# Kernel tuning notes

Hardware: AMD Instinct MI355X
Metric: run time of the kernel (lower is better)

## Reference

```python
import jax, jax.numpy as jnp
import numpy as np

N = 50000
IN_CH = 256
HID = 256
E = 800000


def setup_inputs() -> dict:
    key = jax.random.key(0)
    ks = jax.random.split(key, 12)
    s = 1.0 / np.sqrt(HID)
    return {
        "x": jax.random.normal(ks[0], (N, IN_CH), jnp.float32),
        "edge_index": jax.random.randint(ks[1], (2, E), 0, N, dtype=jnp.int64),
        "prev_embedding": jax.random.normal(ks[2], (N, HID), jnp.float32),
        "W1": jax.random.normal(ks[3], (IN_CH, HID), jnp.float32) / np.sqrt(IN_CH),
        "b1": jnp.zeros((HID,), jnp.float32),
        "W2": jax.random.normal(ks[4], (HID, HID), jnp.float32) * s,
        "b2": jnp.zeros((HID,), jnp.float32),
        "gWw": jax.random.normal(ks[5], (HID, HID), jnp.float32) * s,
        "gWb": jnp.zeros((HID,), jnp.float32),
        "gUw": jax.random.normal(ks[6], (HID, HID), jnp.float32) * s,
        "gUb": jnp.zeros((HID,), jnp.float32),
    }


def _gcn_conv(x, W, b, src, dst, norm):
    # PyG GCNConv: h = x @ W; out[i] = sum_j norm_ij * h[j]; + bias
    h = x @ W
    msg = h[src] * norm[:, None]  # [E+N, H]
    out = jax.ops.segment_sum(msg, dst, num_segments=N)
    return out + b


def _norm_and_loops(edge_index):
    loop = jnp.arange(N, dtype=edge_index.dtype)
    src = jnp.concatenate([edge_index[0], loop])
    dst = jnp.concatenate([edge_index[1], loop])
    deg = jax.ops.segment_sum(jnp.ones_like(dst, dtype=jnp.float32), dst, num_segments=N)
    dinv = jnp.where(deg > 0, jax.lax.rsqrt(deg), 0.0)
    norm = dinv[src] * dinv[dst]
    return src, dst, norm


def reference(x, edge_index, prev_embedding, W1, b1, W2, b2, gWw, gWb, gUw, gUb):
    src, dst, norm = _norm_and_loops(edge_index)
    h = jax.nn.relu(_gcn_conv(x, W1, b1, src, dst, norm))
    h_t = _gcn_conv(h, W2, b2, src, dst, norm)
    alpha = jax.nn.sigmoid(h_t @ gWw + gWb + prev_embedding @ gUw + gUb)
    h_tilde = alpha * h_t + (1.0 - alpha) * prev_embedding
    return (h_tilde, h_t)
```

## Files before the change

kernel.cpp:

```cpp
#include <hip/hip_runtime.h>
#include <hip/hip_bf16.h>
#include <math.h>

#define HIDC 256

typedef short short8 __attribute__((ext_vector_type(8)));
typedef float f32x4 __attribute__((ext_vector_type(4)));

__device__ __forceinline__ ushort f2bf_rne(float f) {
    uint u = __float_as_uint(f);
    u += 0x7FFF + ((u >> 16) & 1);
    return (ushort)(u >> 16);
}
__device__ __forceinline__ float bf2f(ushort h) {
    return __uint_as_float(((uint)h) << 16);
}

__device__ __forceinline__ short8 pack8_rne(float4 a, float4 b) {
    ushort h[8];
    h[0] = f2bf_rne(a.x); h[1] = f2bf_rne(a.y); h[2] = f2bf_rne(a.z); h[3] = f2bf_rne(a.w);
    h[4] = f2bf_rne(b.x); h[5] = f2bf_rne(b.y); h[6] = f2bf_rne(b.z); h[7] = f2bf_rne(b.w);
    return *(short8*)h;
}
__device__ __forceinline__ void split8(float4 a, float4 b, short8& hi, short8& lo) {
    float v[8] = {a.x, a.y, a.z, a.w, b.x, b.y, b.z, b.w};
    ushort hh[8], ll[8];
#pragma unroll
    for (int q = 0; q < 8; q++) {
        uint u = __float_as_uint(v[q]);
        hh[q] = (ushort)(u >> 16);
        ll[q] = f2bf_rne(v[q] - __uint_as_float(u & 0xFFFF0000u));
    }
    hi = *(short8*)hh; lo = *(short8*)ll;
}


__global__ void fill_i_kernel(int* __restrict__ p, int v, int n) {
    int i = blockIdx.x * 256 + threadIdx.x;
    if (i < n) p[i] = v;
}

__global__ void deg_kernel(const int* __restrict__ dst, int* __restrict__ deg, int E) {
    int e = blockIdx.x * 256 + threadIdx.x;
    if (e < E) atomicAdd(&deg[dst[e]], 1);
}

__global__ void rsqrt_kernel(const int* __restrict__ deg, float* __restrict__ dinv, int n) {
    int i = blockIdx.x * 256 + threadIdx.x;
    if (i < n) dinv[i] = rsqrtf((float)(deg[i] + 1));
}


__device__ __forceinline__ int block_incl_scan(int v, int tid) {
#pragma unroll
    for (int off = 1; off < 64; off <<= 1) {
        int t = __shfl_up(v, off);
        if ((tid & 63) >= off) v += t;
    }
    __shared__ int wt[4];
    if ((tid & 63) == 63) wt[tid >> 6] = v;
    __syncthreads();
    int wid = tid >> 6;
    for (int w = 0; w < wid; w++) v += wt[w];
    __syncthreads();
    return v;
}

__global__ void scan_a_kernel(const int* __restrict__ deg, int* __restrict__ row_start,
                              int* __restrict__ blocksum, int N) {
    int tid = threadIdx.x;
    int i = blockIdx.x * 256 + tid;
    int v = (i < N) ? deg[i] : 0;
    int incl = block_incl_scan(v, tid);
    if (i < N) row_start[i + 1] = incl;
    if (tid == 255) blocksum[blockIdx.x] = incl;
}

__global__ void scan_b_kernel(int* __restrict__ blocksum, int nb) {
    int tid = threadIdx.x;
    int v = (tid < nb) ? blocksum[tid] : 0;
    int incl = block_incl_scan(v, tid);
    if (tid < nb) blocksum[tid] = incl;
}

__global__ void scan_c_kernel(int* __restrict__ row_start, int* __restrict__ cursor,
                              const int* __restrict__ blocksum, int N) {
    int b = blockIdx.x;
    int i = b * 256 + threadIdx.x;
    int add = (b > 0) ? blocksum[b - 1] : 0;
    if (i < N) {
        int v = row_start[i + 1] + add;
        row_start[i + 1] = v;
        cursor[i + 1] = v;
    }
    if (b == 0 && threadIdx.x == 0) { row_start[0] = 0; cursor[0] = 0; }
}

__global__ void scatter_kernel(const int* __restrict__ src, const int* __restrict__ dst,
                               const float* __restrict__ dinv, int* __restrict__ cursor,
                               int* __restrict__ csr_src, float* __restrict__ csr_w, int E) {
    int e = blockIdx.x * 256 + threadIdx.x;
    if (e < E) {
        int s = src[e], d = dst[e];
        int pos = atomicAdd(&cursor[d], 1);
        csr_src[pos] = s;
        csr_w[pos] = dinv[s] * dinv[d];
    }
}


__global__ void prep_bt_kernel(const float* __restrict__ B, ushort* __restrict__ BF) {
    int n = blockIdx.x, k = threadIdx.x;
    ushort v = f2bf_rne(B[k * 256 + n]);
    int lane = ((k >> 3) & 3) * 16 + (n & 15);
    int idx = ((n >> 4) * 4096) + ((k >> 5) * 512) + lane * 8 + (k & 7);
    BF[idx] = v;
}

__global__ void prep_gate_bt_kernel(const float* __restrict__ gWw, const float* __restrict__ gUw,
                                    ushort* __restrict__ BhF, ushort* __restrict__ BlF) {
    int n = blockIdx.x, t = threadIdx.x;
#pragma unroll
    for (int p = 0; p < 2; p++) {
        int k = p * 256 + t;
        float v = (p ? gUw : gWw)[t * 256 + n];
        uint u = __float_as_uint(v);
        ushort hi = (ushort)(u >> 16);
        ushort lo = f2bf_rne(v - __uint_as_float(u & 0xFFFF0000u));
        int lane = ((k >> 3) & 3) * 16 + (n & 15);
        int idx = ((n >> 4) * 8192) + ((k >> 5) * 512) + lane * 8 + (k & 7);
        BhF[idx] = hi; BlF[idx] = lo;
    }
}


__global__ __launch_bounds__(256, 4) void gemm_bf16_kernel(
    const float* __restrict__ A, const ushort* __restrict__ BF,
    ushort* __restrict__ C, int M)
{
    const int tl = threadIdx.x;
    const int lane = tl & 63, wave = tl >> 6;
    const int wm = (wave & 1) * 32, wn = (wave >> 1) * 64;
    const int bm = blockIdx.x * 64, bn = blockIdx.y * 128;
    const int fr = lane & 15, kg = (lane >> 4) * 8;

    const int r0 = bm + wm + fr, r1 = r0 + 16;
    const bool ok0 = r0 < M, ok1 = r1 < M;
    const float* a0 = A + (size_t)r0 * HIDC + kg;
    const float* a1 = A + (size_t)r1 * HIDC + kg;
    const ushort* bp = BF + (size_t)((bn + wn) >> 4) * 4096 + lane * 8;

    f32x4 acc[2][4] = {};

    for (int kq = 0; kq < 8; kq++) {
        float4 z = make_float4(0.f, 0.f, 0.f, 0.f);
        float4 u0 = z, u1 = z, v0 = z, v1 = z;
        if (ok0) { u0 = *(const float4*)(a0 + kq * 32); u1 = *(const float4*)(a0 + kq * 32 + 4); }
        if (ok1) { v0 = *(const float4*)(a1 + kq * 32); v1 = *(const float4*)(a1 + kq * 32 + 4); }
        short8 af0 = pack8_rne(u0, u1);
        short8 af1 = pack8_rne(v0, v1);
        short8 bfv[4];
#pragma unroll
        for (int nt = 0; nt < 4; nt++)
            bfv[nt] = *(const short8*)(bp + ((size_t)nt * 8 + kq) * 512);
#pragma unroll
        for (int nt = 0; nt < 4; nt++) {
            acc[0][nt] = __builtin_amdgcn_mfma_f32_16x16x32_bf16(af0, bfv[nt], acc[0][nt], 0, 0, 0);
            acc[1][nt] = __builtin_amdgcn_mfma_f32_16x16x32_bf16(af1, bfv[nt], acc[1][nt], 0, 0, 0);
        }
    }

    const int row4 = (lane >> 4) * 4, coln = lane & 15;
#pragma unroll
    for (int mt = 0; mt < 2; mt++)
#pragma unroll
        for (int r = 0; r < 4; r++) {
            int m = bm + wm + mt * 16 + row4 + r;
            if (m < M) {
#pragma unroll
                for (int nt = 0; nt < 4; nt++) {
                    int n = bn + wn + nt * 16 + coln;
                    C[(size_t)m * HIDC + n] = f2bf_rne(acc[mt][nt][r]);
                }
            }
        }
}


__global__ __launch_bounds__(256, 4) void gemm_bf16A_kernel(
    const ushort* __restrict__ A, const ushort* __restrict__ BF,
    ushort* __restrict__ C, int M)
{
    const int tl = threadIdx.x;
    const int lane = tl & 63, wave = tl >> 6;
    const int wm = (wave & 1) * 32, wn = (wave >> 1) * 64;
    const int bm = blockIdx.x * 64, bn = blockIdx.y * 128;
    const int fr = lane & 15, kg = (lane >> 4) * 8;

    const int r0 = bm + wm + fr, r1 = r0 + 16;
    const bool ok0 = r0 < M, ok1 = r1 < M;
    const ushort* a0 = A + (size_t)r0 * HIDC + kg;
    const ushort* a1 = A + (size_t)r1 * HIDC + kg;
    const ushort* bp = BF + (size_t)((bn + wn) >> 4) * 4096 + lane * 8;

    f32x4 acc[2][4] = {};

    for (int kq = 0; kq < 8; kq++) {
        short8 af0 = {}, af1 = {};
        if (ok0) af0 = *(const short8*)(a0 + kq * 32);
        if (ok1) af1 = *(const short8*)(a1 + kq * 32);
        short8 bfv[4];
#pragma unroll
        for (int nt = 0; nt < 4; nt++)
            bfv[nt] = *(const short8*)(bp + ((size_t)nt * 8 + kq) * 512);
#pragma unroll
        for (int nt = 0; nt < 4; nt++) {
            acc[0][nt] = __builtin_amdgcn_mfma_f32_16x16x32_bf16(af0, bfv[nt], acc[0][nt], 0, 0, 0);
            acc[1][nt] = __builtin_amdgcn_mfma_f32_16x16x32_bf16(af1, bfv[nt], acc[1][nt], 0, 0, 0);
        }
    }

    const int row4 = (lane >> 4) * 4, coln = lane & 15;
#pragma unroll
    for (int mt = 0; mt < 2; mt++)
#pragma unroll
        for (int r = 0; r < 4; r++) {
            int m = bm + wm + mt * 16 + row4 + r;
            if (m < M) {
#pragma unroll
                for (int nt = 0; nt < 4; nt++) {
                    int n = bn + wn + nt * 16 + coln;
                    C[(size_t)m * HIDC + n] = f2bf_rne(acc[mt][nt][r]);
                }
            }
        }
}


__global__ __launch_bounds__(256, 4) void gate_kernel(
    const float* __restrict__ ht, const float* __restrict__ prev,
    const ushort* __restrict__ BhF, const ushort* __restrict__ BlF,
    const float* __restrict__ gWb, const float* __restrict__ gUb,
    float* __restrict__ out, int M)
{
    const int tl = threadIdx.x;
    const int lane = tl & 63, wave = tl >> 6;
    const int wm = (wave & 1) * 32, wn = (wave >> 1) * 64;
    const int bm = blockIdx.x * 64, bn = blockIdx.y * 128;
    const int fr = lane & 15, kg = (lane >> 4) * 8;

    const int r0 = bm + wm + fr, r1 = r0 + 16;
    const bool ok0 = r0 < M, ok1 = r1 < M;
    const size_t ro0 = (size_t)r0 * HIDC + kg;
    const size_t ro1 = (size_t)r1 * HIDC + kg;
    const ushort* bph = BhF + (size_t)((bn + wn) >> 4) * 8192 + lane * 8;
    const ushort* bpl = BlF + (size_t)((bn + wn) >> 4) * 8192 + lane * 8;

    f32x4 acc[2][4] = {};

    for (int kq = 0; kq < 16; kq++) {
        const float* S = (kq < 8) ? ht : prev;
        const int cb = (kq & 7) * 32;
        float4 z = make_float4(0.f, 0.f, 0.f, 0.f);
        float4 u0 = z, u1 = z, v0 = z, v1 = z;
        if (ok0) { u0 = *(const float4*)(S + ro0 + cb); u1 = *(const float4*)(S + ro0 + cb + 4); }
        if (ok1) { v0 = *(const float4*)(S + ro1 + cb); v1 = *(const float4*)(S + ro1 + cb + 4); }
        short8 ah0, al0, ah1, al1;
        split8(u0, u1, ah0, al0);
        split8(v0, v1, ah1, al1);
        short8 bfh[4], bfl[4];
#pragma unroll
        for (int nt = 0; nt < 4; nt++) {
            size_t off = ((size_t)nt * 16 + kq) * 512;
            bfh[nt] = *(const short8*)(bph + off);
            bfl[nt] = *(const short8*)(bpl + off);
        }
#pragma unroll
        for (int nt = 0; nt < 4; nt++) {
            acc[0][nt] = __builtin_amdgcn_mfma_f32_16x16x32_bf16(ah0, bfh[nt], acc[0][nt], 0, 0, 0);
            acc[0][nt] = __builtin_amdgcn_mfma_f32_16x16x32_bf16(ah0, bfl[nt], acc[0][nt], 0, 0, 0);
            acc[0][nt] = __builtin_amdgcn_mfma_f32_16x16x32_bf16(al0, bfh[nt], acc[0][nt], 0, 0, 0);
            acc[1][nt] = __builtin_amdgcn_mfma_f32_16x16x32_bf16(ah1, bfh[nt], acc[1][nt], 0, 0, 0);
            acc[1][nt] = __builtin_amdgcn_mfma_f32_16x16x32_bf16(ah1, bfl[nt], acc[1][nt], 0, 0, 0);
            acc[1][nt] = __builtin_amdgcn_mfma_f32_16x16x32_bf16(al1, bfh[nt], acc[1][nt], 0, 0, 0);
        }
    }

    const int row4 = (lane >> 4) * 4, coln = lane & 15;
#pragma unroll
    for (int mt = 0; mt < 2; mt++)
#pragma unroll
        for (int r = 0; r < 4; r++) {
            int m = bm + wm + mt * 16 + row4 + r;
            if (m < M) {
#pragma unroll
                for (int nt = 0; nt < 4; nt++) {
                    int n = bn + wn + nt * 16 + coln;
                    size_t idx = (size_t)m * HIDC + n;
                    float g = acc[mt][nt][r] + gWb[n] + gUb[n];
                    float alpha = 1.f / (1.f + expf(-g));
                    out[idx] = alpha * ht[idx] + (1.f - alpha) * prev[idx];
                }
            }
        }
}


__global__ __launch_bounds__(256) void csr_agg_kernel(
    const ushort* __restrict__ hm, const int* __restrict__ row_start,
    const int* __restrict__ csr_src, const float* __restrict__ csr_w,
    const float* __restrict__ dinv, const float* __restrict__ bias,
    float* __restrict__ outf, ushort* __restrict__ outb, int do_relu, int N)
{
    const int wave = threadIdx.x >> 6, lane = threadIdx.x & 63;
    const int i = blockIdx.x * 4 + wave;
    if (i >= N) return;
    const int c = lane * 4;

    const float di = dinv[i];
    const float s2 = di * di;
    ushort4 sv = *(const ushort4*)(hm + (size_t)i * HIDC + c);
    float a0 = s2 * bf2f(sv.x), a1 = s2 * bf2f(sv.y);
    float a2 = s2 * bf2f(sv.z), a3 = s2 * bf2f(sv.w);

    const int b0 = row_start[i], b1 = row_start[i + 1];
    int t = b0;
    for (; t + 4 <= b1; t += 4) {
        int   i0 = csr_src[t],     i1 = csr_src[t + 1];
        int   i2 = csr_src[t + 2], i3 = csr_src[t + 3];
        float w0 = csr_w[t],       w1 = csr_w[t + 1];
        float w2 = csr_w[t + 2],   w3 = csr_w[t + 3];
        ushort4 v0 = *(const ushort4*)(hm + (size_t)i0 * HIDC + c);
        ushort4 v1 = *(const ushort4*)(hm + (size_t)i1 * HIDC + c);
        ushort4 v2 = *(const ushort4*)(hm + (size_t)i2 * HIDC + c);
        ushort4 v3 = *(const ushort4*)(hm + (size_t)i3 * HIDC + c);
        a0 += w0 * bf2f(v0.x); a1 += w0 * bf2f(v0.y); a2 += w0 * bf2f(v0.z); a3 += w0 * bf2f(v0.w);
        a0 += w1 * bf2f(v1.x); a1 += w1 * bf2f(v1.y); a2 += w1 * bf2f(v1.z); a3 += w1 * bf2f(v1.w);
        a0 += w2 * bf2f(v2.x); a1 += w2 * bf2f(v2.y); a2 += w2 * bf2f(v2.z); a3 += w2 * bf2f(v2.w);
        a0 += w3 * bf2f(v3.x); a1 += w3 * bf2f(v3.y); a2 += w3 * bf2f(v3.z); a3 += w3 * bf2f(v3.w);
    }
    for (; t < b1; ++t) {
        int s_ = csr_src[t];
        float w = csr_w[t];
        ushort4 v = *(const ushort4*)(hm + (size_t)s_ * HIDC + c);
        a0 += w * bf2f(v.x); a1 += w * bf2f(v.y); a2 += w * bf2f(v.z); a3 += w * bf2f(v.w);
    }

    float4 bb = *(const float4*)(bias + c);
    a0 += bb.x; a1 += bb.y; a2 += bb.z; a3 += bb.w;
    if (do_relu) {
        a0 = fmaxf(a0, 0.f); a1 = fmaxf(a1, 0.f);
        a2 = fmaxf(a2, 0.f); a3 = fmaxf(a3, 0.f);
    }
    if (outb) {
        ushort4 o;
        o.x = f2bf_rne(a0); o.y = f2bf_rne(a1);
        o.z = f2bf_rne(a2); o.w = f2bf_rne(a3);
        *(ushort4*)(outb + (size_t)i * HIDC + c) = o;
    } else {
        *(float4*)(outf + (size_t)i * HIDC + c) = make_float4(a0, a1, a2, a3);
    }
}


extern "C" void kernel_launch(void* const* d_in, const int* in_sizes, int n_in,
                              void* d_out, int out_size, void* d_ws, size_t ws_size,
                              hipStream_t stream) {
    const float* x    = (const float*)d_in[0];
    const int*   ei   = (const int*)d_in[1];
    const float* prev = (const float*)d_in[2];
    const float* W1   = (const float*)d_in[3];
    const float* b1   = (const float*)d_in[4];
    const float* W2   = (const float*)d_in[5];
    const float* b2   = (const float*)d_in[6];
    const float* gWw  = (const float*)d_in[7];
    const float* gWb  = (const float*)d_in[8];
    const float* gUw  = (const float*)d_in[9];
    const float* gUb  = (const float*)d_in[10];

    const int N = in_sizes[0] / HIDC;
    const int E = in_sizes[1] / 2;
    const int* src = ei;
    const int* dst = ei + E;

    float* out  = (float*)d_out;
    float* out1 = out;
    float* ht   = out + (size_t)N * HIDC;
    ushort* hbf = (ushort*)out1;

    float* ws = (float*)d_ws;
    size_t o = 0;
    auto take = [&](size_t n) { size_t r = o; o += (n + 63) & ~(size_t)63; return r; };
    float*  dinv    = ws + take(N);
    int*    degi    = (int*)(ws + take(N));
    int*    row_st  = (int*)(ws + take(N + 1));
    int*    cursor  = (int*)(ws + take(N + 1));
    int*    csr_src = (int*)(ws + take(E));
    float*  csr_w   = ws + take(E);
    ushort* Bt1F    = (ushort*)(ws + take(256 * 256 / 2));
    ushort* Bt2F    = (ushort*)(ws + take(256 * 256 / 2));
    ushort* BthF    = (ushort*)(ws + take(256 * 512 / 2));
    ushort* BtlF    = (ushort*)(ws + take(256 * 512 / 2));
    ushort* hm      = (ushort*)(ws + take((size_t)N * HIDC / 2));

    const int nbN = (N + 255) / 256;
    const int nbE = (E + 255) / 256;
    dim3 ggrid((N + 63) / 64, 2);
    const int nbAgg = (N + 3) / 4;

    int* blocksum = (int*)csr_w;
    fill_i_kernel<<<nbN, 256, 0, stream>>>(degi, 0, N);
    deg_kernel<<<nbE, 256, 0, stream>>>(dst, degi, E);
    scan_a_kernel<<<nbN, 256, 0, stream>>>(degi, row_st, blocksum, N);
    scan_b_kernel<<<1, 256, 0, stream>>>(blocksum, nbN);
    scan_c_kernel<<<nbN, 256, 0, stream>>>(row_st, cursor, blocksum, N);
    rsqrt_kernel<<<nbN, 256, 0, stream>>>(degi, dinv, N);
    scatter_kernel<<<nbE, 256, 0, stream>>>(src, dst, dinv, cursor, csr_src, csr_w, E);

    prep_bt_kernel<<<256, 256, 0, stream>>>(W1, Bt1F);
    prep_bt_kernel<<<256, 256, 0, stream>>>(W2, Bt2F);
    prep_gate_bt_kernel<<<256, 256, 0, stream>>>(gWw, gUw, BthF, BtlF);

    gemm_bf16_kernel<<<ggrid, 256, 0, stream>>>(x, Bt1F, hm, N);
    csr_agg_kernel<<<nbAgg, 256, 0, stream>>>(hm, row_st, csr_src, csr_w, dinv, b1,
                                              nullptr, hbf, 1, N);

    gemm_bf16A_kernel<<<ggrid, 256, 0, stream>>>(hbf, Bt2F, hm, N);
    csr_agg_kernel<<<nbAgg, 256, 0, stream>>>(hm, row_st, csr_src, csr_w, dinv, b2,
                                              ht, nullptr, 0, N);

    gate_kernel<<<ggrid, 256, 0, stream>>>(ht, prev, BthF, BtlF, gWb, gUb, out1, N);

    (void)n_in; (void)out_size; (void)ws_size;
}
```

Baseline: 567.3 us.

## Stage A tiles through double-buffered LDS with register prefetch in GEMM kernels

```diff
diff --git a/kernel.cpp b/kernel.cpp
--- a/kernel.cpp
+++ b/kernel.cpp
@@ -3,6 +3,7 @@
 #include <math.h>
 
 #define HIDC 256
+#define ALD 40
 
 typedef short short8 __attribute__((ext_vector_type(8)));
 typedef float f32x4 __attribute__((ext_vector_type(4)));
@@ -14,6 +15,9 @@
 }
 __device__ __forceinline__ float bf2f(ushort h) {
     return __uint_as_float(((uint)h) << 16);
+}
+__device__ __forceinline__ f32x4 MF(short8 a, short8 b, f32x4 c) {
+    return __builtin_amdgcn_mfma_f32_16x16x32_bf16(a, b, c, 0, 0, 0);
 }
 
 __device__ __forceinline__ short8 pack8_rne(float4 a, float4 b) {
@@ -138,35 +142,53 @@
     const float* __restrict__ A, const ushort* __restrict__ BF,
     ushort* __restrict__ C, int M)
 {
+    __shared__ __align__(16) ushort As[2][64 * ALD];
     const int tl = threadIdx.x;
     const int lane = tl & 63, wave = tl >> 6;
     const int wm = (wave & 1) * 32, wn = (wave >> 1) * 64;
     const int bm = blockIdx.x * 64, bn = blockIdx.y * 128;
-    const int fr = lane & 15, kg = (lane >> 4) * 8;
-
-    const int r0 = bm + wm + fr, r1 = r0 + 16;
-    const bool ok0 = r0 < M, ok1 = r1 < M;
-    const float* a0 = A + (size_t)r0 * HIDC + kg;
-    const float* a1 = A + (size_t)r1 * HIDC + kg;
+    const int fr = lane & 15, koff = (lane >> 4) * 8;
+
+    const int sr = tl >> 2, sc = (tl & 3) * 8;
+    const bool sok = (bm + sr) < M;
+    const float* sp = A + (size_t)(bm + sr) * HIDC + sc;
     const ushort* bp = BF + (size_t)((bn + wn) >> 4) * 4096 + lane * 8;
 
     f32x4 acc[2][4] = {};
-
+    const float4 z4 = make_float4(0.f, 0.f, 0.f, 0.f);
+
+    {
+        float4 u0 = sok ? *(const float4*)(sp)     : z4;
+        float4 u1 = sok ? *(const float4*)(sp + 4) : z4;
+        *(short8*)&As[0][sr * ALD + sc] = pack8_rne(u0, u1);
+    }
+    __syncthreads();
+
+    int cur = 0;
+#pragma unroll
     for (int kq = 0; kq < 8; kq++) {
-        float4 z = make_float4(0.f, 0.f, 0.f, 0.f);
-        float4 u0 = z, u1 = z, v0 = z, v1 = z;
-        if (ok0) { u0 = *(const float4*)(a0 + kq * 32); u1 = *(const float4*)(a0 + kq * 32 + 4); }
-        if (ok1) { v0 = *(const float4*)(a1 + kq * 32); v1 = *(const float4*)(a1 + kq * 32 + 4); }
-        short8 af0 = pack8_rne(u0, u1);
-        short8 af1 = pack8_rne(v0, v1);
+        float4 n0 = z4, n1 = z4;
+        if (kq + 1 < 8 && sok) {
+            n0 = *(const float4*)(sp + (kq + 1) * 32);
+            n1 = *(const float4*)(sp + (kq + 1) * 32 + 4);
+        }
         short8 bfv[4];
 #pragma unroll
         for (int nt = 0; nt < 4; nt++)
             bfv[nt] = *(const short8*)(bp + ((size_t)nt * 8 + kq) * 512);
+        short8 af[2];
+#pragma unroll
+        for (int mt = 0; mt < 2; mt++)
+            af[mt] = *(const short8*)&As[cur][(wm + mt * 16 + fr) * ALD + koff];
 #pragma unroll
         for (int nt = 0; nt < 4; nt++) {
-            acc[0][nt] = __builtin_amdgcn_mfma_f32_16x16x32_bf16(af0, bfv[nt], acc[0][nt], 0, 0, 0);
-            acc[1][nt] = __builtin_amdgcn_mfma_f32_16x16x32_bf16(af1, bfv[nt], acc[1][nt], 0, 0, 0);
+            acc[0][nt] = MF(af[0], bfv[nt], acc[0][nt]);
+            acc[1][nt] = MF(af[1], bfv[nt], acc[1][nt]);
+        }
+        if (kq + 1 < 8) {
+            *(short8*)&As[cur ^ 1][sr * ALD + sc] = pack8_rne(n0, n1);
+            __syncthreads();
+            cur ^= 1;
         }
     }
 
@@ -191,32 +213,49 @@
     const ushort* __restrict__ A, const ushort* __restrict__ BF,
     ushort* __restrict__ C, int M)
 {
+    __shared__ __align__(16) ushort As[2][64 * ALD];
     const int tl = threadIdx.x;
     const int lane = tl & 63, wave = tl >> 6;
     const int wm = (wave & 1) * 32, wn = (wave >> 1) * 64;
     const int bm = blockIdx.x * 64, bn = blockIdx.y * 128;
-    const int fr = lane & 15, kg = (lane >> 4) * 8;
-
-    const int r0 = bm + wm + fr, r1 = r0 + 16;
-    const bool ok0 = r0 < M, ok1 = r1 < M;
-    const ushort* a0 = A + (size_t)r0 * HIDC + kg;
-    const ushort* a1 = A + (size_t)r1 * HIDC + kg;
+    const int fr = lane & 15, koff = (lane >> 4) * 8;
+
+    const int sr = tl >> 2, sc = (tl & 3) * 8;
+    const bool sok = (bm + sr) < M;
+    const ushort* sp = A + (size_t)(bm + sr) * HIDC + sc;
     const ushort* bp = BF + (size_t)((bn + wn) >> 4) * 4096 + lane * 8;
 
     f32x4 acc[2][4] = {};
-
+    const short8 z8 = {};
+
+    {
+        short8 u = sok ? *(const short8*)(sp) : z8;
+        *(short8*)&As[0][sr * ALD + sc] = u;
+    }
+    __syncthreads();
+
+    int cur = 0;
+#pragma unroll
     for (int kq = 0; kq < 8; kq++) {
-        short8 af0 = {}, af1 = {};
-        if (ok0) af0 = *(const short8*)(a0 + kq * 32);
-        if (ok1) af1 = *(const short8*)(a1 + kq * 32);
+        short8 nx = z8;
+        if (kq + 1 < 8 && sok) nx = *(const short8*)(sp + (kq + 1) * 32);
         short8 bfv[4];
 #pragma unroll
         for (int nt = 0; nt < 4; nt++)
             bfv[nt] = *(const short8*)(bp + ((size_t)nt * 8 + kq) * 512);
+        short8 af[2];
+#pragma unroll
+        for (int mt = 0; mt < 2; mt++)
+            af[mt] = *(const short8*)&As[cur][(wm + mt * 16 + fr) * ALD + koff];
 #pragma unroll
         for (int nt = 0; nt < 4; nt++) {
-            acc[0][nt] = __builtin_amdgcn_mfma_f32_16x16x32_bf16(af0, bfv[nt], acc[0][nt], 0, 0, 0);
-            acc[1][nt] = __builtin_amdgcn_mfma_f32_16x16x32_bf16(af1, bfv[nt], acc[1][nt], 0, 0, 0);
+            acc[0][nt] = MF(af[0], bfv[nt], acc[0][nt]);
+            acc[1][nt] = MF(af[1], bfv[nt], acc[1][nt]);
+        }
+        if (kq + 1 < 8) {
+            *(short8*)&As[cur ^ 1][sr * ALD + sc] = nx;
+            __syncthreads();
+            cur ^= 1;
         }
     }
 
@@ -243,46 +282,70 @@
     const float* __restrict__ gWb, const float* __restrict__ gUb,
     float* __restrict__ out, int M)
 {
+    __shared__ __align__(16) ushort Ash[2][64 * ALD];
+    __shared__ __align__(16) ushort Asl[2][64 * ALD];
     const int tl = threadIdx.x;
     const int lane = tl & 63, wave = tl >> 6;
     const int wm = (wave & 1) * 32, wn = (wave >> 1) * 64;
     const int bm = blockIdx.x * 64, bn = blockIdx.y * 128;
-    const int fr = lane & 15, kg = (lane >> 4) * 8;
-
-    const int r0 = bm + wm + fr, r1 = r0 + 16;
-    const bool ok0 = r0 < M, ok1 = r1 < M;
-    const size_t ro0 = (size_t)r0 * HIDC + kg;
-    const size_t ro1 = (size_t)r1 * HIDC + kg;
+    const int fr = lane & 15, koff = (lane >> 4) * 8;
+
+    const int sr = tl >> 2, sc = (tl & 3) * 8;
+    const bool sok = (bm + sr) < M;
+    const size_t sbase = (size_t)(bm + sr) * HIDC + sc;
     const ushort* bph = BhF + (size_t)((bn + wn) >> 4) * 8192 + lane * 8;
     const ushort* bpl = BlF + (size_t)((bn + wn) >> 4) * 8192 + lane * 8;
 
     f32x4 acc[2][4] = {};
-
+    const float4 z4 = make_float4(0.f, 0.f, 0.f, 0.f);
+
+    {
+        float4 u0 = sok ? *(const float4*)(ht + sbase)     : z4;
+        float4 u1 = sok ? *(const float4*)(ht + sbase + 4) : z4;
+        short8 hi, lo; split8(u0, u1, hi, lo);
+        *(short8*)&Ash[0][sr * ALD + sc] = hi;
+        *(short8*)&Asl[0][sr * ALD + sc] = lo;
+    }
+    __syncthreads();
+
+    int cur = 0;
+#pragma unroll
     for (int kq = 0; kq < 16; kq++) {
-        const float* S = (kq < 8) ? ht : prev;
-        const int cb = (kq & 7) * 32;
-        float4 z = make_float4(0.f, 0.f, 0.f, 0.f);
-        float4 u0 = z, u1 = z, v0 = z, v1 = z;
-        if (ok0) { u0 = *(const float4*)(S + ro0 + cb); u1 = *(const float4*)(S + ro0 + cb + 4); }
-        if (ok1) { v0 = *(const float4*)(S + ro1 + cb); v1 = *(const float4*)(S + ro1 + cb + 4); }
-        short8 ah0, al0, ah1, al1;
-        split8(u0, u1, ah0, al0);
-        split8(v0, v1, ah1, al1);
-        short8 bfh[4], bfl[4];
+        float4 n0 = z4, n1 = z4;
+        if (kq + 1 < 16 && sok) {
+            const float* S = ((kq + 1) < 8) ? ht : prev;
+            const int cb = ((kq + 1) & 7) * 32;
+            n0 = *(const float4*)(S + sbase + cb);
+            n1 = *(const float4*)(S + sbase + cb + 4);
+        }
+        short8 bh[4], bl[4];
 #pragma unroll
         for (int nt = 0; nt < 4; nt++) {
             size_t off = ((size_t)nt * 16 + kq) * 512;
-            bfh[nt] = *(const short8*)(bph + off);
-            bfl[nt] = *(const short8*)(bpl + off);
+            bh[nt] = *(const short8*)(bph + off);
+            bl[nt] = *(const short8*)(bpl + off);
+        }
+        short8 ah[2], al[2];
+#pragma unroll
+        for (int mt = 0; mt < 2; mt++) {
+            ah[mt] = *(const short8*)&Ash[cur][(wm + mt * 16 + fr) * ALD + koff];
+            al[mt] = *(const short8*)&Asl[cur][(wm + mt * 16 + fr) * ALD + koff];
         }
 #pragma unroll
         for (int nt = 0; nt < 4; nt++) {
-            acc[0][nt] = __builtin_amdgcn_mfma_f32_16x16x32_bf16(ah0, bfh[nt], acc[0][nt], 0, 0, 0);
-            acc[0][nt] = __builtin_amdgcn_mfma_f32_16x16x32_bf16(ah0, bfl[nt], acc[0][nt], 0, 0, 0);
-            acc[0][nt] = __builtin_amdgcn_mfma_f32_16x16x32_bf16(al0, bfh[nt], acc[0][nt], 0, 0, 0);
-            acc[1][nt] = __builtin_amdgcn_mfma_f32_16x16x32_bf16(ah1, bfh[nt], acc[1][nt], 0, 0, 0);
-            acc[1][nt] = __builtin_amdgcn_mfma_f32_16x16x32_bf16(ah1, bfl[nt], acc[1][nt], 0, 0, 0);
-            acc[1][nt] = __builtin_amdgcn_mfma_f32_16x16x32_bf16(al1, bfh[nt], acc[1][nt], 0, 0, 0);
+            acc[0][nt] = MF(ah[0], bh[nt], acc[0][nt]);
+            acc[0][nt] = MF(ah[0], bl[nt], acc[0][nt]);
+            acc[0][nt] = MF(al[0], bh[nt], acc[0][nt]);
+            acc[1][nt] = MF(ah[1], bh[nt], acc[1][nt]);
+            acc[1][nt] = MF(ah[1], bl[nt], acc[1][nt]);
+            acc[1][nt] = MF(al[1], bh[nt], acc[1][nt]);
+        }
+        if (kq + 1 < 16) {
+            short8 hi, lo; split8(n0, n1, hi, lo);
+            *(short8*)&Ash[cur ^ 1][sr * ALD + sc] = hi;
+            *(short8*)&Asl[cur ^ 1][sr * ALD + sc] = lo;
+            __syncthreads();
+            cur ^= 1;
         }
     }
 
```

After: 523.4 us. -7.8%, faster.
